# Performance work log

Measured on AMD Instinct MI355X. Metric: run time of the kernel, lower is better.

## Reference

```python
import jax, jax.numpy as jnp
import numpy as np


def setup_inputs() -> dict:
    key = jax.random.key(0)
    k1, k2, k3, k4, k5 = jax.random.split(key, 5)
    B, T, R, H = 64, 256, 49, 1024  # batch, caption len, regions (7x7), hidden
    V = jax.random.normal(k1, (B, R, H), dtype=jnp.float32)
    h_t = jax.random.normal(k2, (B, T, H), dtype=jnp.float32)
    Wv = jax.random.normal(k3, (R, H), dtype=jnp.float32) * (1.0 / np.sqrt(H))
    Wg = jax.random.normal(k4, (R, H), dtype=jnp.float32) * (1.0 / np.sqrt(H))
    Wh = jax.random.normal(k5, (1, R), dtype=jnp.float32) * (1.0 / np.sqrt(R))
    return {"V": V, "h_t": h_t, "Wv": Wv, "Wg": Wg, "Wh": Wh}


def reference(V, h_t, Wv, Wg, Wh):
    # content_v: [B,1,R,R] + [B,T,1,R] -> [B,T,R,R]
    cv = jnp.einsum('brh,kh->brk', V, Wv)      # [B, R, R]
    cg = jnp.einsum('bth,kh->btk', h_t, Wg)    # [B, T, R]
    content_v = cv[:, None, :, :] + cg[:, :, None, :]  # [B, T, R, R]
    # z_t = affine_h(tanh(content_v)) squeezed -> [B, T, R]
    z_t = jnp.einsum('btrk,k->btr', jnp.tanh(content_v), Wh[0])
    alpha_t = jax.nn.softmax(z_t, axis=-1)     # [B, T, R]
    c_t = jnp.einsum('btr,brh->bth', alpha_t, V)  # [B, T, H]
    return (c_t, alpha_t)
```

## Files before the change

kernel.cpp:

```cpp
#include <hip/hip_runtime.h>
#include <hip/hip_bf16.h>
#include <math.h>
#include <stdint.h>


typedef __attribute__((ext_vector_type(8))) short bf16x8;
typedef __attribute__((ext_vector_type(4))) short bf16x4;
typedef __attribute__((ext_vector_type(4))) float floatx4;

static __device__ __forceinline__ bf16x8 pack8(float4 a, float4 b) {
    union { __hip_bfloat162 h[4]; bf16x8 v; } u;
    u.h[0] = __float22bfloat162_rn(make_float2(a.x, a.y));
    u.h[1] = __float22bfloat162_rn(make_float2(a.z, a.w));
    u.h[2] = __float22bfloat162_rn(make_float2(b.x, b.y));
    u.h[3] = __float22bfloat162_rn(make_float2(b.z, b.w));
    return u.v;
}

static __device__ __forceinline__ bf16x4 pack4(float4 a) {
    union { __hip_bfloat162 h[2]; bf16x4 v; } u;
    u.h[0] = __float22bfloat162_rn(make_float2(a.x, a.y));
    u.h[1] = __float22bfloat162_rn(make_float2(a.z, a.w));
    return u.v;
}

static __device__ __forceinline__ unsigned short f2bf_bits(float f) {
    union { __hip_bfloat16 h; unsigned short u; } c;
    c.h = __float2bfloat16(f);
    return c.u;
}

__global__ __launch_bounds__(256) void gemm_mfma_tr(const float* __restrict__ Av,
                                                    const float* __restrict__ Ag,
                                                    const float* __restrict__ Wv,
                                                    const float* __restrict__ Wg,
                                                    float* __restrict__ Cv,
                                                    float* __restrict__ Cg,
                                                    unsigned short* __restrict__ vT) {
    __shared__ __align__(16) char smem[20480];
    const int bid = blockIdx.x;
    const int tid = threadIdx.x;

    if (bid >= 1220) {
        float* Ts = (float*)smem;
        const int tb = bid - 1220;
        const int b = tb >> 4;
        const int h0 = (tb & 15) * 64;
        for (int i = tid; i < 49 * 16; i += 256) {
            const int r = i >> 4, hq = i & 15;
            *(float4*)(Ts + r * 68 + hq * 4) =
                *(const float4*)(Av + ((size_t)b * 49 + r) * 1024 + h0 + hq * 4);
        }
        __syncthreads();
        const int h = tid & 63;
        const int grp = tid >> 6;
        float f[16];
#pragma unroll
        for (int j = 0; j < 16; ++j) {
            const int r = grp * 16 + j;
            f[j] = (r < 49) ? Ts[r * 68 + h] : 0.f;
        }
        const size_t rowbase = ((size_t)b * 1024 + h0 + h) * 64;
#pragma unroll
        for (int o2 = 0; o2 < 2; ++o2) {
            const int o = grp * 2 + o2;
            bf16x8 v = pack8(make_float4(f[o2*8+0], f[o2*8+1], f[o2*8+2], f[o2*8+3]),
                             make_float4(f[o2*8+4], f[o2*8+5], f[o2*8+6], f[o2*8+7]));
            *(bf16x8*)(vT + rowbase + (size_t)((o ^ (h & 7)) * 8)) = v;
        }
        return;
    }

    short* As = (short*)smem;
    short* Ws = (short*)(smem + 4096);
    const float* A; const float* W; float* C; int m0;
    if (bid < 196) { A = Av; W = Wv; C = Cv; m0 = bid * 16; }
    else           { A = Ag; W = Wg; C = Cg; m0 = (bid - 196) * 16; }

    const int wave = tid >> 6, lane = tid & 63;
    const int quad = lane >> 4, l16 = lane & 15;
    const int nb = wave * 16;

    floatx4 acc = {};

    const int arow = tid >> 4, ag = tid & 15;
    const int wrow = tid >> 2, wq = tid & 3;
    const float* aptr = A + (size_t)(m0 + arow) * 1024 + ag * 4;
    const bool wvalid = wrow < 49;
    const float* wptr = W + (size_t)wrow * 1024 + wq * 16;
    short* adst = As + arow * 64 + (((ag >> 1) ^ (arow & 7)) * 8) + (ag & 1) * 4;
    short* wdst0 = Ws + wrow * 64;

    float4 ra[2];
    float4 rw[2][4];
    const float4 fz = make_float4(0.f, 0.f, 0.f, 0.f);

    ra[0] = *(const float4*)(aptr);
    if (wvalid) {
        rw[0][0] = *(const float4*)(wptr);
        rw[0][1] = *(const float4*)(wptr + 4);
        rw[0][2] = *(const float4*)(wptr + 8);
        rw[0][3] = *(const float4*)(wptr + 12);
    } else { rw[0][0] = rw[0][1] = rw[0][2] = rw[0][3] = fz; }
    *(bf16x4*)(adst) = pack4(ra[0]);
    *(bf16x8*)(wdst0 + (((wq * 2)     ^ (wrow & 7)) * 8)) = pack8(rw[0][0], rw[0][1]);
    *(bf16x8*)(wdst0 + (((wq * 2 + 1) ^ (wrow & 7)) * 8)) = pack8(rw[0][2], rw[0][3]);
    ra[1] = *(const float4*)(aptr + 64);
    if (wvalid) {
        rw[1][0] = *(const float4*)(wptr + 64);
        rw[1][1] = *(const float4*)(wptr + 68);
        rw[1][2] = *(const float4*)(wptr + 72);
        rw[1][3] = *(const float4*)(wptr + 76);
    } else { rw[1][0] = rw[1][1] = rw[1][2] = rw[1][3] = fz; }
    __syncthreads();

#pragma unroll
    for (int kc = 0; kc < 16; ++kc) {
        const int cur = kc & 1;
        const int curA = cur * 1024, curW = cur * 4096;
        if (kc < 14) {
            const int off = (kc + 2) * 64;
            ra[cur] = *(const float4*)(aptr + off);
            if (wvalid) {
                rw[cur][0] = *(const float4*)(wptr + off);
                rw[cur][1] = *(const float4*)(wptr + off + 4);
                rw[cur][2] = *(const float4*)(wptr + off + 8);
                rw[cur][3] = *(const float4*)(wptr + off + 12);
            }
        }
        {
            const int am = l16;
            const int wn = nb + l16;
            bf16x8 af0 = *(const bf16x8*)(As + curA + am * 64 + ((quad       ^ (am & 7)) * 8));
            bf16x8 af1 = *(const bf16x8*)(As + curA + am * 64 + (((4 + quad) ^ (am & 7)) * 8));
            bf16x8 bf0 = *(const bf16x8*)(Ws + curW + wn * 64 + ((quad       ^ (wn & 7)) * 8));
            bf16x8 bf1 = *(const bf16x8*)(Ws + curW + wn * 64 + (((4 + quad) ^ (wn & 7)) * 8));
            acc = __builtin_amdgcn_mfma_f32_16x16x32_bf16(af0, bf0, acc, 0, 0, 0);
            acc = __builtin_amdgcn_mfma_f32_16x16x32_bf16(af1, bf1, acc, 0, 0, 0);
        }
        if (kc < 15) {
            const int nxt = cur ^ 1;
            const int nA = nxt * 1024, nW = nxt * 4096;
            *(bf16x4*)(adst + nA) = pack4(ra[nxt]);
            *(bf16x8*)(wdst0 + nW + (((wq * 2)     ^ (wrow & 7)) * 8)) = pack8(rw[nxt][0], rw[nxt][1]);
            *(bf16x8*)(wdst0 + nW + (((wq * 2 + 1) ^ (wrow & 7)) * 8)) = pack8(rw[nxt][2], rw[nxt][3]);
        }
        __syncthreads();
    }

    const int n = nb + l16;
    if (n < 49) {
#pragma unroll
        for (int r = 0; r < 4; ++r) {
            const int m = m0 + quad * 4 + r;
            C[(size_t)m * 49 + n] = acc[r];
        }
    }
}

__global__ __launch_bounds__(256) void zsoftmax(const float* __restrict__ cv,
                                                const float* __restrict__ cg,
                                                const float* __restrict__ Wh,
                                                float* __restrict__ alpha,
                                                unsigned short* __restrict__ a16) {
    const int b = blockIdx.x >> 4;
    const int t0 = (blockIdx.x & 15) * 16;
    __shared__ __align__(16) float cvl[49 * 52];
    __shared__ __align__(16) float cgl[16 * 52];
    __shared__ __align__(16) float whl[52];

    const int tid = threadIdx.x;
    for (int i = tid; i < 49 * 49; i += 256) {
        int r = i / 49, k = i - r * 49;
        cvl[r * 52 + k] = cv[(size_t)b * 2401 + i];
    }
    for (int i = tid; i < 16 * 49; i += 256) {
        int t = i / 49, k = i - t * 49;
        cgl[t * 52 + k] = cg[((size_t)b * 256 + t0) * 49 + i];
    }
    if (tid < 52) whl[tid] = (tid < 49) ? Wh[tid] : 0.f;
    __syncthreads();

    const int wave = tid >> 6;
    const int lane = tid & 63;
    const float4* cvr = (const float4*)(cvl + lane * 52);
    const float4* wh4 = (const float4*)whl;

    for (int i = 0; i < 4; ++i) {
        const int tl = wave * 4 + i;
        float z = -INFINITY;
        if (lane < 49) {
            const float4* cgr = (const float4*)(cgl + tl * 52);
            float s = 0.f;
#pragma unroll 4
            for (int kk = 0; kk < 12; ++kk) {
                float4 x = cvr[kk], g = cgr[kk], w = wh4[kk];
                float r0 = __builtin_amdgcn_rcpf(__expf(2.f * (x.x + g.x)) + 1.f);
                float r1 = __builtin_amdgcn_rcpf(__expf(2.f * (x.y + g.y)) + 1.f);
                float r2 = __builtin_amdgcn_rcpf(__expf(2.f * (x.z + g.z)) + 1.f);
                float r3 = __builtin_amdgcn_rcpf(__expf(2.f * (x.w + g.w)) + 1.f);
                s = fmaf(1.f - 2.f * r0, w.x, s);
                s = fmaf(1.f - 2.f * r1, w.y, s);
                s = fmaf(1.f - 2.f * r2, w.z, s);
                s = fmaf(1.f - 2.f * r3, w.w, s);
            }
            {
                float x = cvl[lane * 52 + 48] + cgl[tl * 52 + 48];
                float r0 = __builtin_amdgcn_rcpf(__expf(2.f * x) + 1.f);
                s = fmaf(1.f - 2.f * r0, whl[48], s);
            }
            z = s;
        }
        float m = z;
        for (int off = 32; off; off >>= 1) m = fmaxf(m, __shfl_xor(m, off));
        float p = (lane < 49) ? __expf(z - m) : 0.f;
        float sum = p;
        for (int off = 32; off; off >>= 1) sum += __shfl_xor(sum, off);
        const float val = p * __builtin_amdgcn_rcpf(sum);

        const size_t grow = (size_t)b * 256 + t0 + tl;
        if (lane < 49) alpha[grow * 49 + lane] = val;
        const int pos = (((lane >> 3) ^ (tl & 7)) << 3) | (lane & 7);
        a16[grow * 64 + pos] = f2bf_bits(val);
    }
}

__global__ __launch_bounds__(256) void ct_mfma(const unsigned short* __restrict__ a16,
                                               const unsigned short* __restrict__ vT,
                                               float* __restrict__ C) {
    const int bid = blockIdx.x;
    const int b = bid >> 5;
    const int t0 = ((bid >> 3) & 3) * 64;
    const int h0 = (bid & 7) * 128;

    __shared__ __align__(16) short Al[64 * 64];
    __shared__ __align__(16) short Vl[128 * 64];

    const int tid = threadIdx.x;
    {
        const bf16x8* src = (const bf16x8*)(a16 + ((size_t)b * 256 + t0) * 64);
        bf16x8* dst = (bf16x8*)Al;
#pragma unroll
        for (int p = 0; p < 2; ++p) dst[tid + p * 256] = src[tid + p * 256];
    }
    {
        const bf16x8* src = (const bf16x8*)(vT + ((size_t)b * 1024 + h0) * 64);
        bf16x8* dst = (bf16x8*)Vl;
#pragma unroll
        for (int p = 0; p < 4; ++p) dst[tid + p * 256] = src[tid + p * 256];
    }
    __syncthreads();

    const int wave = tid >> 6, lane = tid & 63;
    const int quad = lane >> 4, l16 = lane & 15;
    const int tb = (wave & 1) * 32;
    const int hb = (wave >> 1) * 64;

    floatx4 acc[2][4] = {};
#pragma unroll
    for (int kc = 0; kc < 2; ++kc) {
        bf16x8 af[2];
#pragma unroll
        for (int ms = 0; ms < 2; ++ms) {
            const int row = tb + ms * 16 + l16;
            af[ms] = *(const bf16x8*)(Al + row * 64 + (((kc << 2) + quad) ^ (row & 7)) * 8);
        }
#pragma unroll
        for (int ns = 0; ns < 4; ++ns) {
            const int row = hb + ns * 16 + l16;
            bf16x8 bf = *(const bf16x8*)(Vl + row * 64 + (((kc << 2) + quad) ^ (row & 7)) * 8);
#pragma unroll
            for (int ms = 0; ms < 2; ++ms)
                acc[ms][ns] = __builtin_amdgcn_mfma_f32_16x16x32_bf16(af[ms], bf, acc[ms][ns], 0, 0, 0);
        }
    }

#pragma unroll
    for (int ms = 0; ms < 2; ++ms) {
        const int t = t0 + tb + ms * 16 + quad * 4;
#pragma unroll
        for (int ns = 0; ns < 4; ++ns) {
            const int h = h0 + hb + ns * 16 + l16;
#pragma unroll
            for (int r = 0; r < 4; ++r)
                C[((size_t)b * 256 + t + r) * 1024 + h] = acc[ms][ns][r];
        }
    }
}

extern "C" void kernel_launch(void* const* d_in, const int* in_sizes, int n_in,
                              void* d_out, int out_size, void* d_ws, size_t ws_size,
                              hipStream_t stream) {
    const float* V   = (const float*)d_in[0];
    const float* h_t = (const float*)d_in[1];
    const float* Wv  = (const float*)d_in[2];
    const float* Wg  = (const float*)d_in[3];
    const float* Wh  = (const float*)d_in[4];

    float* c_t   = (float*)d_out;
    float* alpha = (float*)d_out + 16777216;

    float* cv = (float*)d_ws;
    float* cg = cv + 153664;
    unsigned short* a16 = (unsigned short*)((char*)d_ws + 3825920);
    unsigned short* vT  = a16 + 16384 * 64;

    gemm_mfma_tr<<<196 + 1024 + 1024, 256, 0, stream>>>(V, h_t, Wv, Wg, cv, cg, vT);
    zsoftmax<<<1024, 256, 0, stream>>>(cv, cg, Wh, alpha, a16);
    ct_mfma<<<2048, 256, 0, stream>>>(a16, vT, c_t);
}
```

Before: 183.9 us.

## Pre-convert weights to bf16 and use register-direct single-wave MFMA GEMM

Splits the fused GEMM+transpose kernel into a prep kernel that converts Wv/Wg to bf16 and builds the transposed V, followed by a 64-thread GEMM. The GEMM drops shared memory and barriers, loading A and the bf16 weights straight into registers with a 4-deep prefetch ring. Each wave computes all 64 output columns across four accumulators, so the fp32-to-bf16 packing of the A tile happens once per wave instead of once per block. The cost is an extra kernel launch and serialization between prep and GEMM, plus possibly lower latency hiding with small single-wave blocks.

After: 185.8 us. No clear change (+1.0%).

```diff
diff --git a/kernel.cpp b/kernel.cpp
--- a/kernel.cpp
+++ b/kernel.cpp
@@ -17,143 +17,124 @@
     return u.v;
 }
 
-static __device__ __forceinline__ bf16x4 pack4(float4 a) {
-    union { __hip_bfloat162 h[2]; bf16x4 v; } u;
-    u.h[0] = __float22bfloat162_rn(make_float2(a.x, a.y));
-    u.h[1] = __float22bfloat162_rn(make_float2(a.z, a.w));
-    return u.v;
-}
-
 static __device__ __forceinline__ unsigned short f2bf_bits(float f) {
     union { __hip_bfloat16 h; unsigned short u; } c;
     c.h = __float2bfloat16(f);
     return c.u;
 }
 
-__global__ __launch_bounds__(256) void gemm_mfma_tr(const float* __restrict__ Av,
-                                                    const float* __restrict__ Ag,
-                                                    const float* __restrict__ Wv,
-                                                    const float* __restrict__ Wg,
-                                                    float* __restrict__ Cv,
-                                                    float* __restrict__ Cg,
-                                                    unsigned short* __restrict__ vT) {
-    __shared__ __align__(16) char smem[20480];
+__global__ __launch_bounds__(256) void prep(const float* __restrict__ V,
+                                            const float* __restrict__ Wv,
+                                            const float* __restrict__ Wg,
+                                            unsigned short* __restrict__ wv16,
+                                            unsigned short* __restrict__ wg16,
+                                            unsigned short* __restrict__ vT) {
     const int bid = blockIdx.x;
     const int tid = threadIdx.x;
 
-    if (bid >= 1220) {
-        float* Ts = (float*)smem;
-        const int tb = bid - 1220;
-        const int b = tb >> 4;
-        const int h0 = (tb & 15) * 64;
-        for (int i = tid; i < 49 * 16; i += 256) {
-            const int r = i >> 4, hq = i & 15;
-            *(float4*)(Ts + r * 68 + hq * 4) =
-                *(const float4*)(Av + ((size_t)b * 49 + r) * 1024 + h0 + hq * 4);
-        }
-        __syncthreads();
-        const int h = tid & 63;
-        const int grp = tid >> 6;
-        float f[16];
-#pragma unroll
-        for (int j = 0; j < 16; ++j) {
-            const int r = grp * 16 + j;
-            f[j] = (r < 49) ? Ts[r * 68 + h] : 0.f;
-        }
-        const size_t rowbase = ((size_t)b * 1024 + h0 + h) * 64;
-#pragma unroll
-        for (int o2 = 0; o2 < 2; ++o2) {
-            const int o = grp * 2 + o2;
-            bf16x8 v = pack8(make_float4(f[o2*8+0], f[o2*8+1], f[o2*8+2], f[o2*8+3]),
-                             make_float4(f[o2*8+4], f[o2*8+5], f[o2*8+6], f[o2*8+7]));
-            *(bf16x8*)(vT + rowbase + (size_t)((o ^ (h & 7)) * 8)) = v;
-        }
+    if (bid < 32) {
+        const float* W = (bid < 16) ? Wv : Wg;
+        unsigned short* O = (bid < 16) ? wv16 : wg16;
+        const int r = (bid & 15) * 4 + (tid >> 6);
+        const int kb = (tid & 63) * 16;
+        float4 f0, f1, f2, f3;
+        if (r < 49) {
+            const float* p = W + (size_t)r * 1024 + kb;
+            f0 = *(const float4*)(p);
+            f1 = *(const float4*)(p + 4);
+            f2 = *(const float4*)(p + 8);
+            f3 = *(const float4*)(p + 12);
+        } else {
+            f0 = f1 = f2 = f3 = make_float4(0.f, 0.f, 0.f, 0.f);
+        }
+        unsigned short* o = O + (size_t)r * 1024 + kb;
+        *(bf16x8*)(o) = pack8(f0, f1);
+        *(bf16x8*)(o + 8) = pack8(f2, f3);
         return;
     }
 
-    short* As = (short*)smem;
-    short* Ws = (short*)(smem + 4096);
-    const float* A; const float* W; float* C; int m0;
-    if (bid < 196) { A = Av; W = Wv; C = Cv; m0 = bid * 16; }
-    else           { A = Ag; W = Wg; C = Cg; m0 = (bid - 196) * 16; }
-
-    const int wave = tid >> 6, lane = tid & 63;
-    const int quad = lane >> 4, l16 = lane & 15;
-    const int nb = wave * 16;
-
-    floatx4 acc = {};
-
-    const int arow = tid >> 4, ag = tid & 15;
-    const int wrow = tid >> 2, wq = tid & 3;
-    const float* aptr = A + (size_t)(m0 + arow) * 1024 + ag * 4;
-    const bool wvalid = wrow < 49;
-    const float* wptr = W + (size_t)wrow * 1024 + wq * 16;
-    short* adst = As + arow * 64 + (((ag >> 1) ^ (arow & 7)) * 8) + (ag & 1) * 4;
-    short* wdst0 = Ws + wrow * 64;
-
-    float4 ra[2];
-    float4 rw[2][4];
-    const float4 fz = make_float4(0.f, 0.f, 0.f, 0.f);
-
-    ra[0] = *(const float4*)(aptr);
-    if (wvalid) {
-        rw[0][0] = *(const float4*)(wptr);
-        rw[0][1] = *(const float4*)(wptr + 4);
-        rw[0][2] = *(const float4*)(wptr + 8);
-        rw[0][3] = *(const float4*)(wptr + 12);
-    } else { rw[0][0] = rw[0][1] = rw[0][2] = rw[0][3] = fz; }
-    *(bf16x4*)(adst) = pack4(ra[0]);
-    *(bf16x8*)(wdst0 + (((wq * 2)     ^ (wrow & 7)) * 8)) = pack8(rw[0][0], rw[0][1]);
-    *(bf16x8*)(wdst0 + (((wq * 2 + 1) ^ (wrow & 7)) * 8)) = pack8(rw[0][2], rw[0][3]);
-    ra[1] = *(const float4*)(aptr + 64);
-    if (wvalid) {
-        rw[1][0] = *(const float4*)(wptr + 64);
-        rw[1][1] = *(const float4*)(wptr + 68);
-        rw[1][2] = *(const float4*)(wptr + 72);
-        rw[1][3] = *(const float4*)(wptr + 76);
-    } else { rw[1][0] = rw[1][1] = rw[1][2] = rw[1][3] = fz; }
+    __shared__ __align__(16) float Ts[49 * 68];
+    const int tb = bid - 32;
+    const int b = tb >> 4;
+    const int h0 = (tb & 15) * 64;
+    for (int i = tid; i < 49 * 16; i += 256) {
+        const int r = i >> 4, hq = i & 15;
+        *(float4*)(Ts + r * 68 + hq * 4) =
+            *(const float4*)(V + ((size_t)b * 49 + r) * 1024 + h0 + hq * 4);
+    }
     __syncthreads();
-
-#pragma unroll
-    for (int kc = 0; kc < 16; ++kc) {
-        const int cur = kc & 1;
-        const int curA = cur * 1024, curW = cur * 4096;
-        if (kc < 14) {
-            const int off = (kc + 2) * 64;
-            ra[cur] = *(const float4*)(aptr + off);
-            if (wvalid) {
-                rw[cur][0] = *(const float4*)(wptr + off);
-                rw[cur][1] = *(const float4*)(wptr + off + 4);
-                rw[cur][2] = *(const float4*)(wptr + off + 8);
-                rw[cur][3] = *(const float4*)(wptr + off + 12);
-            }
-        }
-        {
-            const int am = l16;
-            const int wn = nb + l16;
-            bf16x8 af0 = *(const bf16x8*)(As + curA + am * 64 + ((quad       ^ (am & 7)) * 8));
-            bf16x8 af1 = *(const bf16x8*)(As + curA + am * 64 + (((4 + quad) ^ (am & 7)) * 8));
-            bf16x8 bf0 = *(const bf16x8*)(Ws + curW + wn * 64 + ((quad       ^ (wn & 7)) * 8));
-            bf16x8 bf1 = *(const bf16x8*)(Ws + curW + wn * 64 + (((4 + quad) ^ (wn & 7)) * 8));
-            acc = __builtin_amdgcn_mfma_f32_16x16x32_bf16(af0, bf0, acc, 0, 0, 0);
-            acc = __builtin_amdgcn_mfma_f32_16x16x32_bf16(af1, bf1, acc, 0, 0, 0);
-        }
-        if (kc < 15) {
-            const int nxt = cur ^ 1;
-            const int nA = nxt * 1024, nW = nxt * 4096;
-            *(bf16x4*)(adst + nA) = pack4(ra[nxt]);
-            *(bf16x8*)(wdst0 + nW + (((wq * 2)     ^ (wrow & 7)) * 8)) = pack8(rw[nxt][0], rw[nxt][1]);
-            *(bf16x8*)(wdst0 + nW + (((wq * 2 + 1) ^ (wrow & 7)) * 8)) = pack8(rw[nxt][2], rw[nxt][3]);
-        }
-        __syncthreads();
-    }
-
-    const int n = nb + l16;
-    if (n < 49) {
-#pragma unroll
-        for (int r = 0; r < 4; ++r) {
-            const int m = m0 + quad * 4 + r;
-            C[(size_t)m * 49 + n] = acc[r];
+    const int h = tid & 63;
+    const int grp = tid >> 6;
+    float f[16];
+#pragma unroll
+    for (int j = 0; j < 16; ++j) {
+        const int r = grp * 16 + j;
+        f[j] = (r < 49) ? Ts[r * 68 + h] : 0.f;
+    }
+    const size_t rowbase = ((size_t)b * 1024 + h0 + h) * 64;
+#pragma unroll
+    for (int o2 = 0; o2 < 2; ++o2) {
+        const int o = grp * 2 + o2;
+        bf16x8 v = pack8(make_float4(f[o2*8+0], f[o2*8+1], f[o2*8+2], f[o2*8+3]),
+                         make_float4(f[o2*8+4], f[o2*8+5], f[o2*8+6], f[o2*8+7]));
+        *(bf16x8*)(vT + rowbase + (size_t)((o ^ (h & 7)) * 8)) = v;
+    }
+}
+
+__global__ __launch_bounds__(64) void gemm_direct(const float* __restrict__ Av,
+                                                  const float* __restrict__ Ag,
+                                                  const unsigned short* __restrict__ wv16,
+                                                  const unsigned short* __restrict__ wg16,
+                                                  float* __restrict__ Cv,
+                                                  float* __restrict__ Cg) {
+    const int bid = blockIdx.x;
+    const int lane = threadIdx.x;
+    const int l16 = lane & 15, quad = lane >> 4;
+
+    const float* A; const unsigned short* W; float* C; int m0;
+    if (bid < 196) { A = Av;  W = wv16; C = Cv; m0 = bid * 16; }
+    else           { A = Ag;  W = wg16; C = Cg; m0 = (bid - 196) * 16; }
+
+    const float* aptr = A + (size_t)(m0 + l16) * 1024 + quad * 8;
+    const unsigned short* bptr = W + (size_t)l16 * 1024 + quad * 8;
+
+    floatx4 acc[4] = {};
+    float4 ra0[4], ra1[4];
+    bf16x8 rb[4][4];
+
+#pragma unroll
+    for (int s = 0; s < 4; ++s) {
+        ra0[s] = *(const float4*)(aptr + s * 32);
+        ra1[s] = *(const float4*)(aptr + s * 32 + 4);
+#pragma unroll
+        for (int j = 0; j < 4; ++j)
+            rb[s][j] = *(const bf16x8*)(bptr + j * 16384 + s * 32);
+    }
+
+#pragma unroll
+    for (int s = 0; s < 32; ++s) {
+        const int slot = s & 3;
+        bf16x8 af = pack8(ra0[slot], ra1[slot]);
+#pragma unroll
+        for (int j = 0; j < 4; ++j)
+            acc[j] = __builtin_amdgcn_mfma_f32_16x16x32_bf16(af, rb[slot][j], acc[j], 0, 0, 0);
+        if (s < 28) {
+            const int k = (s + 4) * 32;
+            ra0[slot] = *(const float4*)(aptr + k);
+            ra1[slot] = *(const float4*)(aptr + k + 4);
+#pragma unroll
+            for (int j = 0; j < 4; ++j)
+                rb[slot][j] = *(const bf16x8*)(bptr + j * 16384 + k);
+        }
+    }
+
+#pragma unroll
+    for (int j = 0; j < 4; ++j) {
+        const int n = j * 16 + l16;
+        if (n < 49) {
+#pragma unroll
+            for (int r = 0; r < 4; ++r)
+                C[(size_t)(m0 + quad * 4 + r) * 49 + n] = acc[j][r];
         }
     }
 }
@@ -302,10 +283,13 @@
 
     float* cv = (float*)d_ws;
     float* cg = cv + 153664;
-    unsigned short* a16 = (unsigned short*)((char*)d_ws + 3825920);
-    unsigned short* vT  = a16 + 16384 * 64;
-
-    gemm_mfma_tr<<<196 + 1024 + 1024, 256, 0, stream>>>(V, h_t, Wv, Wg, cv, cg, vT);
+    unsigned short* a16  = (unsigned short*)((char*)d_ws + 3825920);
+    unsigned short* vT   = a16 + 16384 * 64;
+    unsigned short* wv16 = vT + (size_t)64 * 1024 * 64;
+    unsigned short* wg16 = wv16 + 64 * 1024;
+
+    prep<<<32 + 1024, 256, 0, stream>>>(V, Wv, Wg, wv16, wg16, vT);
+    gemm_direct<<<196 + 1024, 64, 0, stream>>>(V, h_t, wv16, wg16, cv, cg);
     zsoftmax<<<1024, 256, 0, stream>>>(cv, cg, Wh, alpha, a16);
     ct_mfma<<<2048, 256, 0, stream>>>(a16, vT, c_t);
 }
```
